# Performance work log

Measured on AMD Instinct MI355X. Metric: run time of the kernel, lower is better.

The kernel has to match this reference:

```python
import jax, jax.numpy as jnp
import numpy as np

B = 16          # graphs per batch (equal-sized, contiguous)
N_PER = 16384   # nodes per graph
N = B * N_PER   # 262144 total nodes
E = 524288      # total edges
D_IN = 128
D_OUT = 128
RATIO = 0.5
K = int(N_PER * RATIO)  # nodes kept per graph by TopKPooling
NEG_SLOPE = 0.01        # F.leaky_relu default


def setup_inputs() -> dict:
    key = jax.random.key(0)
    ks = jax.random.split(key, 7)
    x = jax.random.normal(ks[0], (N, D_IN), jnp.float32)
    # edges constrained within each graph so per-graph pooling is meaningful
    e_per = E // B
    off = (jnp.arange(B, dtype=jnp.int32) * N_PER)[:, None]
    src = jax.random.randint(ks[1], (B, e_per), 0, N_PER, dtype=jnp.int32) + off
    dst = jax.random.randint(ks[2], (B, e_per), 0, N_PER, dtype=jnp.int32) + off
    edge_index = jnp.stack([src.reshape(-1), dst.reshape(-1)], axis=0)
    edge_weight = jax.random.uniform(ks[3], (E,), jnp.float32)
    batch = jnp.repeat(jnp.arange(B, dtype=jnp.int32), N_PER)
    conv_weight = jax.random.normal(ks[4], (D_IN, D_OUT), jnp.float32) / np.sqrt(D_IN)
    conv_bias = jnp.zeros((D_OUT,), jnp.float32)
    pool_weight = jax.random.normal(ks[5], (D_OUT,), jnp.float32)
    return {"x": x, "edge_index": edge_index, "edge_weight": edge_weight,
            "batch": batch, "conv_weight": conv_weight, "conv_bias": conv_bias,
            "pool_weight": pool_weight}


def reference(x, edge_index, edge_weight, batch, conv_weight, conv_bias, pool_weight):
    # Dropout is identity in eval mode (p=0.0).
    row, col = edge_index[0], edge_index[1]

    # ---- GCNConv: gcn_norm with added self-loops (fill_value=1) ----
    loop = jnp.arange(N, dtype=row.dtype)
    row_sl = jnp.concatenate([row, loop])
    col_sl = jnp.concatenate([col, loop])
    w_sl = jnp.concatenate([edge_weight, jnp.ones((N,), edge_weight.dtype)])
    deg = jax.ops.segment_sum(w_sl, col_sl, num_segments=N)          # in-degree at targets
    dinv = jnp.where(deg > 0, jax.lax.rsqrt(deg), 0.0)
    norm = dinv[row_sl] * w_sl * dinv[col_sl]                        # [E+N]

    xw = x @ conv_weight                                             # [N, D_OUT]
    msgs = norm[:, None] * xw[row_sl]                                # gather at sources
    h = jax.ops.segment_sum(msgs, col_sl, num_segments=N) + conv_bias  # scatter-add at targets
    h = jax.nn.leaky_relu(h, NEG_SLOPE)

    # ---- TopKPooling: score = tanh(x . w / ||w||), keep top K per graph ----
    score = jnp.tanh((h @ pool_weight) / jnp.linalg.norm(pool_weight))  # [N]
    _, idx = jax.lax.top_k(score.reshape(B, N_PER), K)                  # [B, K] local idx
    perm = (idx + (jnp.arange(B, dtype=idx.dtype) * N_PER)[:, None]).reshape(-1)  # [B*K]

    x_out = h[perm] * score[perm][:, None]                              # gate kept nodes
    batch_new = batch[perm]

    # ---- filter_adj: relabel, keep edges whose both endpoints survive ----
    mapping = jnp.full((N,), -1, dtype=row.dtype).at[perm].set(
        jnp.arange(B * K, dtype=row.dtype))
    r2, c2 = mapping[row], mapping[col]
    valid = (r2 >= 0) & (c2 >= 0)
    edge_index_new = jnp.where(valid, jnp.stack([r2, c2], axis=0), 0)   # padded (static shape)
    edge_weight_new = jnp.where(valid, edge_weight, 0.0)
    return x_out, edge_index_new, edge_weight_new, batch_new
```

## Files before the change

kernel.cpp:

```cpp
#include <hip/hip_runtime.h>
#include <math.h>

#define N_NODES 262144
#define N_EDGES 524288
#define NB      16
#define N_PER   16384
#define KKEEP   8192
#define DIM     128
#define NEG_SLOPE 0.01f
#define CHUNK   2048

#define X_OUT   0
#define X_EI    16777216
#define X_EW    17825792
#define X_BATCH 18350080

typedef short s8v __attribute__((ext_vector_type(8)));
typedef float f4v __attribute__((ext_vector_type(4)));

__device__ __forceinline__ unsigned long long pack_key(float sc, int localIdx) {
    unsigned int u = __float_as_uint(sc);
    u = (u & 0x80000000u) ? ~u : (u | 0x80000000u);
    unsigned int inv = ~u;
    return ((unsigned long long)inv << 32) | (unsigned int)localIdx;
}

__device__ __forceinline__ unsigned int f2bf(float x) {
    unsigned int u = __float_as_uint(x);
    return (u + 0x7FFFu + ((u >> 16) & 1u)) >> 16;
}
__device__ __forceinline__ float bf2f(unsigned int h) { return __uint_as_float(h << 16); }

__global__ void k_init(float* deg, int* count, int* mapping, const float* pw, float* normPw) {
    int n = blockIdx.x * 256 + threadIdx.x;
    if (n < N_NODES) { deg[n] = 1.0f; count[n] = 0; mapping[n] = -1; }
    if (n == 0) {
        float s = 0.f;
        for (int i = 0; i < DIM; i++) s += pw[i] * pw[i];
        normPw[0] = sqrtf(s);
    }
}

__global__ void k_wprep(const float* Wg, unsigned short* Wt0, unsigned short* Wt1,
                        unsigned short* Wt2) {
    int idx = blockIdx.x * 256 + threadIdx.x;
    if (idx >= DIM * DIM) return;
    int k = idx >> 7, n = idx & 127;
    float wv = Wg[k * 128 + n];
    unsigned int h = f2bf(wv);
    float r1 = wv - bf2f(h);
    unsigned int m = f2bf(r1);
    float r2 = r1 - bf2f(m);
    unsigned int lo = f2bf(r2);
    Wt0[n * 128 + k] = (unsigned short)h;
    Wt1[n * 128 + k] = (unsigned short)m;
    Wt2[n * 128 + k] = (unsigned short)lo;
}

__global__ void k_deg(const int* col, const float* w, float* deg, int* count) {
    int e = blockIdx.x * 256 + threadIdx.x;
    if (e >= N_EDGES) return;
    int c = col[e];
    atomicAdd(&deg[c], w[e]);
    atomicAdd(&count[c], 1);
}

__global__ void k_scan1(const int* count, int* offs, int* blockSums) {
    __shared__ int s[2048];
    int base = blockIdx.x * 2048;
    int t = threadIdx.x;
    s[t]        = count[base + t];
    s[t + 1024] = count[base + t + 1024];
    __syncthreads();
    for (int off = 1; off < 2048; off <<= 1) {
        int a0 = (t >= off)        ? s[t - off]        : 0;
        int a1 = (t + 1024 >= off) ? s[t + 1024 - off] : 0;
        __syncthreads();
        s[t]        += a0;
        s[t + 1024] += a1;
        __syncthreads();
    }
    offs[base + t]        = s[t]        - count[base + t];
    offs[base + t + 1024] = s[t + 1024] - count[base + t + 1024];
    if (t == 0) blockSums[blockIdx.x] = s[2047];
}

__global__ void k_scan2(int* blockSums, int* offs) {
    if (threadIdx.x == 0) {
        int run = 0;
        for (int b = 0; b < 128; b++) { int v = blockSums[b]; blockSums[b] = run; run += v; }
        offs[N_NODES] = run;
    }
}

__global__ void k_fixup(int* offs, int* count, float* deg, const int* blockSums) {
    int n = blockIdx.x * 256 + threadIdx.x;
    if (n >= N_NODES) return;
    offs[n] += blockSums[n >> 11];
    count[n] = 0;
    float d = deg[n];
    deg[n] = (d > 0.f) ? (1.0f / sqrtf(d)) : 0.f;
}

__global__ void k_scatter(const int* row, const int* col, const float* w, const float* dinv,
                          const int* offs, int* cursor, int* ssrc, float* scoef) {
    int e = blockIdx.x * 256 + threadIdx.x;
    if (e >= N_EDGES) return;
    int r = row[e], c = col[e];
    int pos = atomicAdd(&cursor[c], 1);
    int slot = offs[c] + pos;
    ssrc[slot]  = r;
    scoef[slot] = (dinv[r] * w[e]) * dinv[c];
}

__global__ void k_aggregate(const float* x, const float* dinv, const int* offs,
                            const int* ssrc, const float* scoef, float* agg) {
    int g = blockIdx.x * 256 + threadIdx.x;
    int node = g >> 5, d = g & 31;
    const float4* x4 = (const float4*)x;
    int s = offs[node], e = offs[node + 1];

    float4 vs = x4[(size_t)node * 32 + d];
    float di = dinv[node];

    float4 acc = make_float4(0.f, 0.f, 0.f, 0.f);
    int j = s;
    while (j + 4 <= e) {
        int   s0 = ssrc[j],  s1 = ssrc[j + 1],  s2 = ssrc[j + 2],  s3 = ssrc[j + 3];
        float c0 = scoef[j], c1 = scoef[j + 1], c2 = scoef[j + 2], c3 = scoef[j + 3];
        float4 va = x4[(size_t)s0 * 32 + d];
        float4 vb = x4[(size_t)s1 * 32 + d];
        float4 vc = x4[(size_t)s2 * 32 + d];
        float4 vd = x4[(size_t)s3 * 32 + d];
        acc.x += c0 * va.x; acc.y += c0 * va.y; acc.z += c0 * va.z; acc.w += c0 * va.w;
        acc.x += c1 * vb.x; acc.y += c1 * vb.y; acc.z += c1 * vb.z; acc.w += c1 * vb.w;
        acc.x += c2 * vc.x; acc.y += c2 * vc.y; acc.z += c2 * vc.z; acc.w += c2 * vc.w;
        acc.x += c3 * vd.x; acc.y += c3 * vd.y; acc.z += c3 * vd.z; acc.w += c3 * vd.w;
        j += 4;
    }
    if (j + 2 <= e) {
        int   s0 = ssrc[j],  s1 = ssrc[j + 1];
        float c0 = scoef[j], c1 = scoef[j + 1];
        float4 va = x4[(size_t)s0 * 32 + d];
        float4 vb = x4[(size_t)s1 * 32 + d];
        acc.x += c0 * va.x; acc.y += c0 * va.y; acc.z += c0 * va.z; acc.w += c0 * va.w;
        acc.x += c1 * vb.x; acc.y += c1 * vb.y; acc.z += c1 * vb.z; acc.w += c1 * vb.w;
        j += 2;
    }
    if (j < e) {
        int   s0 = ssrc[j];
        float c0 = scoef[j];
        float4 va = x4[(size_t)s0 * 32 + d];
        acc.x += c0 * va.x; acc.y += c0 * va.y; acc.z += c0 * va.z; acc.w += c0 * va.w;
    }
    float cf = di * di;
    acc.x += cf * vs.x; acc.y += cf * vs.y; acc.z += cf * vs.z; acc.w += cf * vs.w;
    ((float4*)agg)[(size_t)node * 32 + d] = acc;
}

__global__ __launch_bounds__(256, 2) void k_gemm(float* hio,
                                                 const unsigned short* Wt0,
                                                 const unsigned short* Wt1,
                                                 const unsigned short* Wt2,
                                                 const float* bias, const float* pw,
                                                 const float* normPw, float* score) {
    __shared__ __align__(16) char smem[49152];
    char* sA0 = smem;
    char* sA1 = smem + 8192;
    char* sA2 = smem + 16384;
    char* sW0 = smem + 24576;
    char* sW1 = smem + 32768;
    char* sW2 = smem + 40960;

    int tid = threadIdx.x;
    int l   = tid & 63;
    int w   = tid >> 6;
    int l15 = l & 15, l4 = l >> 4;
    int row0 = blockIdx.x * 128;

    f4v acc[2][8];
#pragma unroll
    for (int mt = 0; mt < 2; mt++)
#pragma unroll
        for (int nt = 0; nt < 8; nt++)
#pragma unroll
            for (int r = 0; r < 4; r++) acc[mt][nt][r] = 0.f;

    for (int kh = 0; kh < 4; kh++) {
        if (kh) __syncthreads();
#pragma unroll
        for (int i = 0; i < 2; i++) {
            int f = tid + i * 256;
            int r = f >> 2, c = f & 3;
            const float* src = hio + (size_t)(row0 + r) * 128 + kh * 32 + c * 8;
            float4 v0 = *(const float4*)(src);
            float4 v1 = *(const float4*)(src + 4);
            float a[8] = {v0.x, v0.y, v0.z, v0.w, v1.x, v1.y, v1.z, v1.w};
            unsigned int h[8], m[8], lo[8];
#pragma unroll
            for (int j = 0; j < 8; j++) {
                h[j] = f2bf(a[j]);
                float r1 = a[j] - bf2f(h[j]);
                m[j] = f2bf(r1);
                float r2 = r1 - bf2f(m[j]);
                lo[j] = f2bf(r2);
            }
            int off = r * 64 + ((c ^ ((r >> 1) & 3)) * 16);
            *(uint4*)(sA0 + off) = make_uint4(h[0] | (h[1] << 16), h[2] | (h[3] << 16),
                                              h[4] | (h[5] << 16), h[6] | (h[7] << 16));
            *(uint4*)(sA1 + off) = make_uint4(m[0] | (m[1] << 16), m[2] | (m[3] << 16),
                                              m[4] | (m[5] << 16), m[6] | (m[7] << 16));
            *(uint4*)(sA2 + off) = make_uint4(lo[0] | (lo[1] << 16), lo[2] | (lo[3] << 16),
                                              lo[4] | (lo[5] << 16), lo[6] | (lo[7] << 16));
        }
#pragma unroll
        for (int i = 0; i < 2; i++) {
            int f = tid + i * 256;
            int n = f >> 2, c = f & 3;
            size_t gb = (size_t)n * 256 + kh * 64 + c * 16;
            int off = n * 64 + ((c ^ ((n >> 1) & 3)) * 16);
            *(uint4*)(sW0 + off) = *(const uint4*)((const char*)Wt0 + gb);
            *(uint4*)(sW1 + off) = *(const uint4*)((const char*)Wt1 + gb);
            *(uint4*)(sW2 + off) = *(const uint4*)((const char*)Wt2 + gb);
        }
        __syncthreads();

        s8v ah[2], am[2], al[2];
#pragma unroll
        for (int mt = 0; mt < 2; mt++) {
            int r = w * 32 + mt * 16 + l15;
            int off = r * 64 + ((l4 ^ ((r >> 1) & 3)) * 16);
            ah[mt] = *(const s8v*)(sA0 + off);
            am[mt] = *(const s8v*)(sA1 + off);
            al[mt] = *(const s8v*)(sA2 + off);
        }
#pragma unroll
        for (int nt = 0; nt < 8; nt++) {
            int rn = nt * 16 + l15;
            int offb = rn * 64 + ((l4 ^ ((rn >> 1) & 3)) * 16);
            s8v b0 = *(const s8v*)(sW0 + offb);
            s8v b1 = *(const s8v*)(sW1 + offb);
            s8v b2 = *(const s8v*)(sW2 + offb);
#pragma unroll
            for (int mt = 0; mt < 2; mt++) {
                acc[mt][nt] = __builtin_amdgcn_mfma_f32_16x16x32_bf16(ah[mt], b0, acc[mt][nt], 0, 0, 0);
                acc[mt][nt] = __builtin_amdgcn_mfma_f32_16x16x32_bf16(ah[mt], b1, acc[mt][nt], 0, 0, 0);
                acc[mt][nt] = __builtin_amdgcn_mfma_f32_16x16x32_bf16(am[mt], b0, acc[mt][nt], 0, 0, 0);
                acc[mt][nt] = __builtin_amdgcn_mfma_f32_16x16x32_bf16(am[mt], b1, acc[mt][nt], 0, 0, 0);
                acc[mt][nt] = __builtin_amdgcn_mfma_f32_16x16x32_bf16(ah[mt], b2, acc[mt][nt], 0, 0, 0);
                acc[mt][nt] = __builtin_amdgcn_mfma_f32_16x16x32_bf16(al[mt], b0, acc[mt][nt], 0, 0, 0);
                acc[mt][nt] = __builtin_amdgcn_mfma_f32_16x16x32_bf16(am[mt], b2, acc[mt][nt], 0, 0, 0);
                acc[mt][nt] = __builtin_amdgcn_mfma_f32_16x16x32_bf16(al[mt], b1, acc[mt][nt], 0, 0, 0);
            }
        }
    }

    float bv[8], pv[8];
#pragma unroll
    for (int nt = 0; nt < 8; nt++) {
        bv[nt] = bias[nt * 16 + l15];
        pv[nt] = pw[nt * 16 + l15];
    }
    float nrm = normPw[0];
    float sp[2][4];
#pragma unroll
    for (int mt = 0; mt < 2; mt++)
#pragma unroll
        for (int r = 0; r < 4; r++) sp[mt][r] = 0.f;

#pragma unroll
    for (int mt = 0; mt < 2; mt++) {
#pragma unroll
        for (int r = 0; r < 4; r++) {
            int row = row0 + w * 32 + mt * 16 + l4 * 4 + r;
#pragma unroll
            for (int nt = 0; nt < 8; nt++) {
                float v = acc[mt][nt][r] + bv[nt];
                v = (v >= 0.f) ? v : NEG_SLOPE * v;
                hio[(size_t)row * 128 + nt * 16 + l15] = v;
                sp[mt][r] += v * pv[nt];
            }
        }
    }
#pragma unroll
    for (int m = 1; m < 16; m <<= 1) {
#pragma unroll
        for (int mt = 0; mt < 2; mt++)
#pragma unroll
            for (int r = 0; r < 4; r++) sp[mt][r] += __shfl_xor(sp[mt][r], m, 64);
    }
    if (l15 == 0) {
#pragma unroll
        for (int mt = 0; mt < 2; mt++)
#pragma unroll
            for (int r = 0; r < 4; r++) {
                int row = row0 + w * 32 + mt * 16 + l4 * 4 + r;
                score[row] = tanhf(sp[mt][r] / nrm);
            }
    }
}

__global__ void __launch_bounds__(1024) k_sortchunks(const float* score,
                                                     unsigned long long* keys) {
    __shared__ unsigned long long a[CHUNK];
    int base = blockIdx.x * CHUNK;
    int t = threadIdx.x;
#pragma unroll
    for (int i = 0; i < CHUNK / 1024; i++) {
        int p = t + i * 1024;
        int node = base + p;
        a[p] = pack_key(score[node], node & (N_PER - 1));
    }
    __syncthreads();
    for (int k = 2; k <= CHUNK; k <<= 1) {
        for (int j = k >> 1; j > 0; j >>= 1) {
#pragma unroll
            for (int q = 0; q < CHUNK / 2048; q++) {
                int tt = t + q * 1024;
                int i = ((tt & ~(j - 1)) << 1) | (tt & (j - 1));
                int l = i | j;
                bool asc = ((i & k) == 0);
                unsigned long long x = a[i], y = a[l];
                if ((x > y) == asc) { a[i] = y; a[l] = x; }
            }
            __syncthreads();
        }
    }
#pragma unroll
    for (int i = 0; i < CHUNK / 1024; i++) {
        int p = t + i * 1024;
        keys[base + p] = a[p];
    }
}

__global__ void k_rank(const float* score, const unsigned long long* keys,
                       int* perm, int* mapping, float* out) {
    int n = blockIdx.x * 256 + threadIdx.x;
    if (n >= N_NODES) return;
    int g = n >> 14;
    unsigned long long key = pack_key(score[n], n & (N_PER - 1));
    const unsigned long long* gb = keys + ((size_t)g << 14);
    int r = 0;
#pragma unroll
    for (int c = 0; c < N_PER / CHUNK; c++) {
        const unsigned long long* ch = gb + c * CHUNK;
        int lo = 0, hi = CHUNK;
        while (lo < hi) {
            int mid = (lo + hi) >> 1;
            if (ch[mid] < key) lo = mid + 1; else hi = mid;
        }
        r += lo;
    }
    if (r < KKEEP) {
        int i = (g << 13) + r;
        perm[i] = n;
        mapping[n] = i;
        out[X_BATCH + i] = (float)g;
    }
}

__global__ void k_gate(const float* h, const float* score, const int* perm, float* out) {
    int g = blockIdx.x * 256 + threadIdx.x;
    int i = g >> 5, d = g & 31;
    int node = perm[i];
    float sc = score[node];
    float4 v = ((const float4*)h)[(size_t)node * 32 + d];
    v.x *= sc; v.y *= sc; v.z *= sc; v.w *= sc;
    ((float4*)(out + X_OUT))[(size_t)i * 32 + d] = v;
}

__global__ void k_edges(const int* row, const int* col, const float* w,
                        const int* mapping, float* out) {
    int e = blockIdx.x * 256 + threadIdx.x;
    if (e >= N_EDGES) return;
    int mr = mapping[row[e]], mc = mapping[col[e]];
    bool valid = (mr >= 0) && (mc >= 0);
    out[X_EI + e]           = valid ? (float)mr : 0.f;
    out[X_EI + N_EDGES + e] = valid ? (float)mc : 0.f;
    out[X_EW + e]           = valid ? w[e] : 0.f;
}

extern "C" void kernel_launch(void* const* d_in, const int* in_sizes, int n_in,
                              void* d_out, int out_size, void* d_ws, size_t ws_size,
                              hipStream_t stream) {
    const float* x     = (const float*)d_in[0];
    const int*   ei    = (const int*)d_in[1];
    const float* ew    = (const float*)d_in[2];
    const float* Wc    = (const float*)d_in[4];
    const float* bias  = (const float*)d_in[5];
    const float* pw    = (const float*)d_in[6];
    float* out = (float*)d_out;

    const int* rowp = ei;
    const int* colp = ei + N_EDGES;

    char* wsb = (char*)d_ws;
    float* agg     = (float*)(wsb);
    float* dinv    = (float*)(wsb + 134217728);
    int*   count   = (int*)  (wsb + 135266304);
    int*   offs    = (int*)  (wsb + 136314880);
    int*   ssrc    = (int*)  (wsb + 137363712);
    float* scoef   = (float*)(wsb + 139460864);
    float* score   = (float*)(wsb + 141557760);
    unsigned long long* keys = (unsigned long long*)(wsb + 142606336);
    int*   perm    = (int*)  (wsb + 144703488);
    int*   mapping = (int*)  (wsb + 145227776);
    int*   blockSums = (int*)(wsb + 146276352);
    float* normPw  = (float*)(wsb + 146277376);
    unsigned short* Wt0 = (unsigned short*)(wsb + 146278400);
    unsigned short* Wt1 = (unsigned short*)(wsb + 146311168);
    unsigned short* Wt2 = (unsigned short*)(wsb + 146343936);

    k_init   <<<N_NODES / 256, 256, 0, stream>>>(dinv, count, mapping, pw, normPw);
    k_wprep  <<<64, 256, 0, stream>>>(Wc, Wt0, Wt1, Wt2);
    k_deg    <<<N_EDGES / 256, 256, 0, stream>>>(colp, ew, dinv, count);
    k_scan1  <<<128, 1024, 0, stream>>>(count, offs, blockSums);
    k_scan2  <<<1, 64, 0, stream>>>(blockSums, offs);
    k_fixup  <<<N_NODES / 256, 256, 0, stream>>>(offs, count, dinv, blockSums);
    k_scatter<<<N_EDGES / 256, 256, 0, stream>>>(rowp, colp, ew, dinv, offs, count, ssrc, scoef);
    k_aggregate<<<(N_NODES * 32) / 256, 256, 0, stream>>>(x, dinv, offs, ssrc, scoef, agg);
    k_gemm   <<<N_NODES / 128, 256, 0, stream>>>(agg, Wt0, Wt1, Wt2, bias, pw, normPw, score);
    k_sortchunks<<<N_NODES / CHUNK, 1024, 0, stream>>>(score, keys);
    k_rank   <<<N_NODES / 256, 256, 0, stream>>>(score, keys, perm, mapping, out);
    k_gate   <<<(NB * KKEEP * 32) / 256, 256, 0, stream>>>(agg, score, perm, out);
    k_edges  <<<N_EDGES / 256, 256, 0, stream>>>(rowp, colp, ew, mapping, out);
}
```

Baseline: 495.2 us.

## Load GEMM operands directly from global into MFMA registers, dropping LDS staging

```diff
diff --git a/kernel.cpp b/kernel.cpp
--- a/kernel.cpp
+++ b/kernel.cpp
@@ -164,20 +164,18 @@
                                                  const unsigned short* Wt2,
                                                  const float* bias, const float* pw,
                                                  const float* normPw, float* score) {
-    __shared__ __align__(16) char smem[49152];
-    char* sA0 = smem;
-    char* sA1 = smem + 8192;
-    char* sA2 = smem + 16384;
-    char* sW0 = smem + 24576;
-    char* sW1 = smem + 32768;
-    char* sW2 = smem + 40960;
-
     int tid = threadIdx.x;
     int l   = tid & 63;
     int w   = tid >> 6;
     int l15 = l & 15, l4 = l >> 4;
     int row0 = blockIdx.x * 128;
 
+    const float* aBase0 = hio + (size_t)(row0 + w * 32 + l15) * 128 + l4 * 8;
+    const float* aBase1 = aBase0 + 16 * 128;
+    const char* w0b = (const char*)Wt0 + (size_t)l15 * 256 + l4 * 16;
+    const char* w1b = (const char*)Wt1 + (size_t)l15 * 256 + l4 * 16;
+    const char* w2b = (const char*)Wt2 + (size_t)l15 * 256 + l4 * 16;
+
     f4v acc[2][8];
 #pragma unroll
     for (int mt = 0; mt < 2; mt++)
@@ -186,61 +184,47 @@
 #pragma unroll
             for (int r = 0; r < 4; r++) acc[mt][nt][r] = 0.f;
 
+    float4 a00 = *(const float4*)(aBase0);
+    float4 a01 = *(const float4*)(aBase0 + 4);
+    float4 a10 = *(const float4*)(aBase1);
+    float4 a11 = *(const float4*)(aBase1 + 4);
+
+#pragma unroll
     for (int kh = 0; kh < 4; kh++) {
-        if (kh) __syncthreads();
-#pragma unroll
-        for (int i = 0; i < 2; i++) {
-            int f = tid + i * 256;
-            int r = f >> 2, c = f & 3;
-            const float* src = hio + (size_t)(row0 + r) * 128 + kh * 32 + c * 8;
-            float4 v0 = *(const float4*)(src);
-            float4 v1 = *(const float4*)(src + 4);
-            float a[8] = {v0.x, v0.y, v0.z, v0.w, v1.x, v1.y, v1.z, v1.w};
-            unsigned int h[8], m[8], lo[8];
+        s8v ah[2], am[2], al[2];
+        {
+            float av0[8] = {a00.x, a00.y, a00.z, a00.w, a01.x, a01.y, a01.z, a01.w};
+            float av1[8] = {a10.x, a10.y, a10.z, a10.w, a11.x, a11.y, a11.z, a11.w};
 #pragma unroll
             for (int j = 0; j < 8; j++) {
-                h[j] = f2bf(a[j]);
-                float r1 = a[j] - bf2f(h[j]);
-                m[j] = f2bf(r1);
-                float r2 = r1 - bf2f(m[j]);
-                lo[j] = f2bf(r2);
+                unsigned int h0 = f2bf(av0[j]);
+                float r10 = av0[j] - bf2f(h0);
+                unsigned int m0 = f2bf(r10);
+                float r20 = r10 - bf2f(m0);
+                unsigned int lo0 = f2bf(r20);
+                ah[0][j] = (short)h0; am[0][j] = (short)m0; al[0][j] = (short)lo0;
+                unsigned int h1 = f2bf(av1[j]);
+                float r11 = av1[j] - bf2f(h1);
+                unsigned int m1 = f2bf(r11);
+                float r21 = r11 - bf2f(m1);
+                unsigned int lo1 = f2bf(r21);
+                ah[1][j] = (short)h1; am[1][j] = (short)m1; al[1][j] = (short)lo1;
             }
-            int off = r * 64 + ((c ^ ((r >> 1) & 3)) * 16);
-            *(uint4*)(sA0 + off) = make_uint4(h[0] | (h[1] << 16), h[2] | (h[3] << 16),
-                                              h[4] | (h[5] << 16), h[6] | (h[7] << 16));
-            *(uint4*)(sA1 + off) = make_uint4(m[0] | (m[1] << 16), m[2] | (m[3] << 16),
-                                              m[4] | (m[5] << 16), m[6] | (m[7] << 16));
-            *(uint4*)(sA2 + off) = make_uint4(lo[0] | (lo[1] << 16), lo[2] | (lo[3] << 16),
-                                              lo[4] | (lo[5] << 16), lo[6] | (lo[7] << 16));
-        }
-#pragma unroll
-        for (int i = 0; i < 2; i++) {
-            int f = tid + i * 256;
-            int n = f >> 2, c = f & 3;
-            size_t gb = (size_t)n * 256 + kh * 64 + c * 16;
-            int off = n * 64 + ((c ^ ((n >> 1) & 3)) * 16);
-            *(uint4*)(sW0 + off) = *(const uint4*)((const char*)Wt0 + gb);
-            *(uint4*)(sW1 + off) = *(const uint4*)((const char*)Wt1 + gb);
-            *(uint4*)(sW2 + off) = *(const uint4*)((const char*)Wt2 + gb);
-        }
-        __syncthreads();
-
-        s8v ah[2], am[2], al[2];
-#pragma unroll
-        for (int mt = 0; mt < 2; mt++) {
-            int r = w * 32 + mt * 16 + l15;
-            int off = r * 64 + ((l4 ^ ((r >> 1) & 3)) * 16);
-            ah[mt] = *(const s8v*)(sA0 + off);
-            am[mt] = *(const s8v*)(sA1 + off);
-            al[mt] = *(const s8v*)(sA2 + off);
+        }
+        if (kh < 3) {
+            const float* p0 = aBase0 + (kh + 1) * 32;
+            const float* p1 = aBase1 + (kh + 1) * 32;
+            a00 = *(const float4*)(p0);
+            a01 = *(const float4*)(p0 + 4);
+            a10 = *(const float4*)(p1);
+            a11 = *(const float4*)(p1 + 4);
         }
 #pragma unroll
         for (int nt = 0; nt < 8; nt++) {
-            int rn = nt * 16 + l15;
-            int offb = rn * 64 + ((l4 ^ ((rn >> 1) & 3)) * 16);
-            s8v b0 = *(const s8v*)(sW0 + offb);
-            s8v b1 = *(const s8v*)(sW1 + offb);
-            s8v b2 = *(const s8v*)(sW2 + offb);
+            size_t bo = (size_t)nt * 4096 + kh * 64;
+            s8v b0 = *(const s8v*)(w0b + bo);
+            s8v b1 = *(const s8v*)(w1b + bo);
+            s8v b2 = *(const s8v*)(w2b + bo);
 #pragma unroll
             for (int mt = 0; mt < 2; mt++) {
                 acc[mt][nt] = __builtin_amdgcn_mfma_f32_16x16x32_bf16(ah[mt], b0, acc[mt][nt], 0, 0, 0);
```

After: 544.8 us. +10.0%, slower.

## Register-prefetch next K-slice of A and W tiles during MFMA loop

Applied to the files above, without the earlier changes.

```diff
diff --git a/kernel.cpp b/kernel.cpp
--- a/kernel.cpp
+++ b/kernel.cpp
@@ -186,44 +186,70 @@
 #pragma unroll
             for (int r = 0; r < 4; r++) acc[mt][nt][r] = 0.f;
 
+    uint4 aPk[2][3];
+    uint4 wPk[2][3];
+
+#pragma unroll
+    for (int i = 0; i < 2; i++) {
+        int f = tid + i * 256;
+        int r = f >> 2, c = f & 3;
+        const float* src = hio + (size_t)(row0 + r) * 128 + 0 * 32 + c * 8;
+        float4 v0 = *(const float4*)(src);
+        float4 v1 = *(const float4*)(src + 4);
+        float a[8] = {v0.x, v0.y, v0.z, v0.w, v1.x, v1.y, v1.z, v1.w};
+        unsigned int h[8], m[8], lo[8];
+#pragma unroll
+        for (int j = 0; j < 8; j++) {
+            h[j] = f2bf(a[j]);
+            float r1 = a[j] - bf2f(h[j]);
+            m[j] = f2bf(r1);
+            float r2 = r1 - bf2f(m[j]);
+            lo[j] = f2bf(r2);
+        }
+        aPk[i][0] = make_uint4(h[0] | (h[1] << 16), h[2] | (h[3] << 16),
+                               h[4] | (h[5] << 16), h[6] | (h[7] << 16));
+        aPk[i][1] = make_uint4(m[0] | (m[1] << 16), m[2] | (m[3] << 16),
+                               m[4] | (m[5] << 16), m[6] | (m[7] << 16));
+        aPk[i][2] = make_uint4(lo[0] | (lo[1] << 16), lo[2] | (lo[3] << 16),
+                               lo[4] | (lo[5] << 16), lo[6] | (lo[7] << 16));
+        size_t gb = (size_t)r * 256 + 0 * 64 + c * 16;
+        wPk[i][0] = *(const uint4*)((const char*)Wt0 + gb);
+        wPk[i][1] = *(const uint4*)((const char*)Wt1 + gb);
+        wPk[i][2] = *(const uint4*)((const char*)Wt2 + gb);
+    }
+
+#pragma unroll
     for (int kh = 0; kh < 4; kh++) {
-        if (kh) __syncthreads();
 #pragma unroll
         for (int i = 0; i < 2; i++) {
             int f = tid + i * 256;
             int r = f >> 2, c = f & 3;
-            const float* src = hio + (size_t)(row0 + r) * 128 + kh * 32 + c * 8;
-            float4 v0 = *(const float4*)(src);
-            float4 v1 = *(const float4*)(src + 4);
-            float a[8] = {v0.x, v0.y, v0.z, v0.w, v1.x, v1.y, v1.z, v1.w};
-            unsigned int h[8], m[8], lo[8];
-#pragma unroll
-            for (int j = 0; j < 8; j++) {
-                h[j] = f2bf(a[j]);
-                float r1 = a[j] - bf2f(h[j]);
-                m[j] = f2bf(r1);
-                float r2 = r1 - bf2f(m[j]);
-                lo[j] = f2bf(r2);
-            }
             int off = r * 64 + ((c ^ ((r >> 1) & 3)) * 16);
-            *(uint4*)(sA0 + off) = make_uint4(h[0] | (h[1] << 16), h[2] | (h[3] << 16),
-                                              h[4] | (h[5] << 16), h[6] | (h[7] << 16));
-            *(uint4*)(sA1 + off) = make_uint4(m[0] | (m[1] << 16), m[2] | (m[3] << 16),
-                                              m[4] | (m[5] << 16), m[6] | (m[7] << 16));
-            *(uint4*)(sA2 + off) = make_uint4(lo[0] | (lo[1] << 16), lo[2] | (lo[3] << 16),
-                                              lo[4] | (lo[5] << 16), lo[6] | (lo[7] << 16));
-        }
-#pragma unroll
-        for (int i = 0; i < 2; i++) {
-            int f = tid + i * 256;
-            int n = f >> 2, c = f & 3;
-            size_t gb = (size_t)n * 256 + kh * 64 + c * 16;
-            int off = n * 64 + ((c ^ ((n >> 1) & 3)) * 16);
-            *(uint4*)(sW0 + off) = *(const uint4*)((const char*)Wt0 + gb);
-            *(uint4*)(sW1 + off) = *(const uint4*)((const char*)Wt1 + gb);
-            *(uint4*)(sW2 + off) = *(const uint4*)((const char*)Wt2 + gb);
+            *(uint4*)(sA0 + off) = aPk[i][0];
+            *(uint4*)(sA1 + off) = aPk[i][1];
+            *(uint4*)(sA2 + off) = aPk[i][2];
+            *(uint4*)(sW0 + off) = wPk[i][0];
+            *(uint4*)(sW1 + off) = wPk[i][1];
+            *(uint4*)(sW2 + off) = wPk[i][2];
         }
         __syncthreads();
+
+        float4 aR[2][2];
+        uint4  wR[2][3];
+        if (kh < 3) {
+#pragma unroll
+            for (int i = 0; i < 2; i++) {
+                int f = tid + i * 256;
+                int r = f >> 2, c = f & 3;
+                const float* src = hio + (size_t)(row0 + r) * 128 + (kh + 1) * 32 + c * 8;
+                aR[i][0] = *(const float4*)(src);
+                aR[i][1] = *(const float4*)(src + 4);
+                size_t gb = (size_t)r * 256 + (kh + 1) * 64 + c * 16;
+                wR[i][0] = *(const uint4*)((const char*)Wt0 + gb);
+                wR[i][1] = *(const uint4*)((const char*)Wt1 + gb);
+                wR[i][2] = *(const uint4*)((const char*)Wt2 + gb);
+            }
+        }
 
         s8v ah[2], am[2], al[2];
 #pragma unroll
@@ -253,6 +279,33 @@
                 acc[mt][nt] = __builtin_amdgcn_mfma_f32_16x16x32_bf16(al[mt], b1, acc[mt][nt], 0, 0, 0);
             }
         }
+
+        if (kh < 3) {
+#pragma unroll
+            for (int i = 0; i < 2; i++) {
+                float a[8] = {aR[i][0].x, aR[i][0].y, aR[i][0].z, aR[i][0].w,
+                              aR[i][1].x, aR[i][1].y, aR[i][1].z, aR[i][1].w};
+                unsigned int h[8], m[8], lo[8];
+#pragma unroll
+                for (int j = 0; j < 8; j++) {
+                    h[j] = f2bf(a[j]);
+                    float r1 = a[j] - bf2f(h[j]);
+                    m[j] = f2bf(r1);
+                    float r2 = r1 - bf2f(m[j]);
+                    lo[j] = f2bf(r2);
+                }
+                aPk[i][0] = make_uint4(h[0] | (h[1] << 16), h[2] | (h[3] << 16),
+                                       h[4] | (h[5] << 16), h[6] | (h[7] << 16));
+                aPk[i][1] = make_uint4(m[0] | (m[1] << 16), m[2] | (m[3] << 16),
+                                       m[4] | (m[5] << 16), m[6] | (m[7] << 16));
+                aPk[i][2] = make_uint4(lo[0] | (lo[1] << 16), lo[2] | (lo[3] << 16),
+                                       lo[4] | (lo[5] << 16), lo[6] | (lo[7] << 16));
+                wPk[i][0] = wR[i][0];
+                wPk[i][1] = wR[i][1];
+                wPk[i][2] = wR[i][2];
+            }
+        }
+        __syncthreads();
     }
 
     float bv[8], pv[8];
```

Result: slower. 552.5 us (+11.6%).
